# Performance work log

Hardware: AMD Instinct MI355X
Metric: run time of the kernel (lower is better)

## Reference

```python
import jax, jax.numpy as jnp
import numpy as np

B, N, D = 4, 1024, 1024
H, HD, G = 16, 64, 4          # num_heads, dim_heads, num_groups
KVH = H // G                   # kv heads = 4


def setup_inputs() -> dict:
    key = jax.random.key(0)
    ks = jax.random.split(key, 5)
    s = 0.02
    return {
        "x": jax.random.normal(ks[0], (B, N, D), jnp.float32),
        "Wq": jax.random.normal(ks[1], (D, H * HD), jnp.float32) * s,
        "Wkv": jax.random.normal(ks[2], (D, 2 * H * HD // G), jnp.float32) * s,
        "Wg": jax.random.normal(ks[3], (D, H * HD), jnp.float32) * s,
        "bg": jnp.zeros((H * HD,), jnp.float32),
        "Wo": jax.random.normal(ks[4], (H * HD, D), jnp.float32) * s,
    }


def reference(x, Wq, Wkv, Wg, bg, Wo):
    # QKV projections (no bias on q/kv/o; bias on gate)
    q = (x @ Wq).reshape(B, N, H, HD).transpose(0, 2, 1, 3)        # (B,H,N,HD)
    kv = x @ Wkv                                                    # (B,N,2*KVH*HD)
    k, v = jnp.split(kv, 2, axis=-1)
    k = k.reshape(B, N, KVH, HD).transpose(0, 2, 1, 3)             # (B,KVH,N,HD)
    v = v.reshape(B, N, KVH, HD).transpose(0, 2, 1, 3)
    # GQA: repeat_interleave kv heads to match query heads
    k = jnp.repeat(k, G, axis=1)                                    # (B,H,N,HD)
    v = jnp.repeat(v, G, axis=1)
    # scaled dot product attention
    scores = jnp.einsum("bhqd,bhkd->bhqk", q, k) / jnp.sqrt(jnp.float32(HD))
    attn = jax.nn.softmax(scores, axis=-1)
    out = jnp.einsum("bhqk,bhkd->bhqd", attn, v)                    # (B,H,N,HD)
    out = out.transpose(0, 2, 1, 3).reshape(B, N, H * HD)
    # elementwise gate then output projection
    gate = x @ Wg + bg
    return (gate * out) @ Wo
```

## Files before the change

### kernel.cpp

```cpp
#include <hip/hip_runtime.h>
#include <hip/hip_bf16.h>
#include <stdint.h>

#define BB 4
#define NN 1024
#define DD 1024
#define HH 16
#define HDIM 64
#define KVHH 4
#define MM (BB * NN)

typedef __hip_bfloat16 bf16;
typedef __attribute__((ext_vector_type(8))) short bf16x8;
typedef __attribute__((ext_vector_type(4))) short bf16x4;
typedef __attribute__((ext_vector_type(4))) float f32x4;

__device__ __forceinline__ float b2f(unsigned short u) {
  return __uint_as_float(((unsigned)u) << 16);
}
__device__ __forceinline__ unsigned short f2b(float x) {
  bf16 h = __float2bfloat16(x);
  unsigned short u;
  __builtin_memcpy(&u, &h, 2);
  return u;
}
__device__ __forceinline__ f32x4 mfma16(bf16x8 a, bf16x8 b, f32x4 c) {
  return __builtin_amdgcn_mfma_f32_16x16x32_bf16(a, b, c, 0, 0, 0);
}
__device__ __forceinline__ f32x4 mfma16k16(bf16x4 a, bf16x4 b, f32x4 c) {
#if __has_builtin(__builtin_amdgcn_mfma_f32_16x16x16bf16_1k)
  return __builtin_amdgcn_mfma_f32_16x16x16bf16_1k(a, b, c, 0, 0, 0);
#else
  asm("s_nop 1\n\tv_mfma_f32_16x16x16_bf16 %0, %1, %2, %0"
      : "+v"(c)
      : "v"(a), "v"(b));
  return c;
#endif
}
__device__ __forceinline__ bf16x4 vlo(bf16x8 v) {
  return __builtin_shufflevector(v, v, 0, 1, 2, 3);
}
__device__ __forceinline__ bf16x4 vhi(bf16x8 v) {
  return __builtin_shufflevector(v, v, 4, 5, 6, 7);
}
__device__ __forceinline__ void gl_lds16(const short* g, short* l) {
  __builtin_amdgcn_global_load_lds(
      (const __attribute__((address_space(1))) unsigned*)g,
      (__attribute__((address_space(3))) unsigned*)l, 16, 0, 0);
}

__global__ __launch_bounds__(256) void transpose_all(
    const float* __restrict__ Wq, const float* __restrict__ Wkv,
    const float* __restrict__ Wg, const float* __restrict__ Wo,
    const float* __restrict__ bg, const float* __restrict__ x,
    short* __restrict__ WcT, short* __restrict__ WoT,
    float* __restrict__ bias, short* __restrict__ xb) {
  const int z = blockIdx.z;
  if (z == 4) {
    if (blockIdx.y == 0 && blockIdx.x < 10) {
      int i = blockIdx.x * 256 + threadIdx.x;
      if (i < 2560) bias[i] = (i >= 1024 && i < 2048) ? bg[i - 1024] : 0.f;
    }
    return;
  }
  if (z == 5) {
    int base = (blockIdx.y * 16 + blockIdx.x) * 256 + threadIdx.x;
#pragma unroll
    for (int it = 0; it < 16; ++it) {
      int i = base + it * 65536;
      float4 v = *(const float4*)&x[(size_t)i * 4];
      ushort4 o;
      o.x = f2b(v.x); o.y = f2b(v.y); o.z = f2b(v.z); o.w = f2b(v.w);
      *(ushort4*)&xb[(size_t)i * 4] = o;
    }
    return;
  }
  const float* W;
  short* WT;
  int N = 1024;
  const int K = 1024;
  if (z == 0) { W = Wq; WT = WcT; }
  else if (z == 1) { W = Wg; WT = WcT + 1048576; }
  else if (z == 2) {
    W = Wkv; WT = WcT + 2097152; N = 512;
    if (blockIdx.x >= 8) return;
  } else { W = Wo; WT = WoT; }

  __shared__ short T[64 * 68];
  const int tid = threadIdx.x;
  const int n0 = blockIdx.x * 64, k0 = blockIdx.y * 64;
  {
    int i0 = tid >> 4, j4 = (tid & 15) * 4;
#pragma unroll
    for (int ii = 0; ii < 4; ++ii) {
      int i = i0 + 16 * ii;
      float4 w = *(const float4*)&W[(size_t)(k0 + i) * N + n0 + j4];
      ushort4 o;
      o.x = f2b(w.x); o.y = f2b(w.y); o.z = f2b(w.z); o.w = f2b(w.w);
      *(ushort4*)&T[i * 68 + j4] = o;
    }
  }
  __syncthreads();
  {
    int n = tid >> 2, k16 = (tid & 3) * 16;
    short tmp[16];
#pragma unroll
    for (int kk = 0; kk < 16; ++kk) tmp[kk] = T[(k16 + kk) * 68 + n];
    short* dst = WT + (size_t)(n0 + n) * K + k0 + k16;
#pragma unroll
    for (int s = 0; s < 16; s += 4) *(ushort4*)&dst[s] = *(const ushort4*)&tmp[s];
  }
}

__global__ __launch_bounds__(256, 3) void gemm_proj(
    const short* __restrict__ A, const short* __restrict__ WT,
    const float* __restrict__ bias, short* __restrict__ qc,
    short* __restrict__ gc, short* __restrict__ kc, short* __restrict__ vt) {
  __shared__ short As[2][128 * 32];
  __shared__ short Bs[2][128 * 32];
  const int tid = threadIdx.x;
  const int wave = tid >> 6, lane = tid & 63, l15 = lane & 15, quad = lane >> 4;
  const int m0 = blockIdx.y * 128, n0 = blockIdx.x * 128;
  const int wm = (wave & 1) * 64, wn = (wave >> 1) * 64;
  const int arow = tid >> 2, ac = (tid & 3) * 8;
  const short* asrc = A + (size_t)(m0 + arow) * 1024 + ac;
  const short* bsrc = WT + (size_t)(n0 + arow) * 1024 + ac;

  gl_lds16(asrc, &As[0][wave * 512]);
  gl_lds16(asrc + 64 * 1024, &As[0][2048 + wave * 512]);
  gl_lds16(bsrc, &Bs[0][wave * 512]);
  gl_lds16(bsrc + 64 * 1024, &Bs[0][2048 + wave * 512]);

  f32x4 acc[4][4] = {};
  for (int k = 0; k < 32; ++k) {
    const int cur = k & 1;
    __syncthreads();
    if (k < 31) {
      const short* ap = asrc + (k + 1) * 32;
      const short* bp = bsrc + (k + 1) * 32;
      gl_lds16(ap, &As[1 - cur][wave * 512]);
      gl_lds16(ap + 64 * 1024, &As[1 - cur][2048 + wave * 512]);
      gl_lds16(bp, &Bs[1 - cur][wave * 512]);
      gl_lds16(bp + 64 * 1024, &Bs[1 - cur][2048 + wave * 512]);
    }
    bf16x8 af[4], bfr[4];
#pragma unroll
    for (int i = 0; i < 4; ++i)
      af[i] = *(const bf16x8*)&As[cur][(wm + 16 * i + l15) * 32 + quad * 8];
#pragma unroll
    for (int j = 0; j < 4; ++j)
      bfr[j] = *(const bf16x8*)&Bs[cur][(wn + 16 * j + l15) * 32 + quad * 8];
#pragma unroll
    for (int i = 0; i < 4; ++i)
#pragma unroll
      for (int j = 0; j < 4; ++j) acc[i][j] = mfma16(af[i], bfr[j], acc[i][j]);
  }

  const int reg = (n0 + wn) >> 6;
  if (reg < 16) {
#pragma unroll
    for (int j = 0; j < 4; ++j) {
      int d = 16 * j + l15;
#pragma unroll
      for (int i = 0; i < 4; ++i)
#pragma unroll
        for (int r = 0; r < 4; ++r) {
          int row = m0 + wm + 16 * i + quad * 4 + r;
          int b = row >> 10, tok = row & 1023;
          ((unsigned short*)qc)[((size_t)((b * 16 + reg) * 1024 + tok)) * 64 + d] =
              f2b(acc[i][j][r] * 0.18033688f);
        }
    }
  } else if (reg < 32) {
#pragma unroll
    for (int j = 0; j < 4; ++j) {
      int d = 16 * j + l15;
      float bv = bias[n0 + wn + d];
#pragma unroll
      for (int i = 0; i < 4; ++i)
#pragma unroll
        for (int r = 0; r < 4; ++r) {
          int row = m0 + wm + 16 * i + quad * 4 + r;
          int b = row >> 10, tok = row & 1023;
          ((unsigned short*)gc)[((size_t)((b * 16 + reg - 16) * 1024 + tok)) * 64 + d] =
              f2b(acc[i][j][r] + bv);
        }
    }
  } else if (reg < 36) {
    int kvh = reg - 32;
#pragma unroll
    for (int j = 0; j < 4; ++j) {
      int d = 16 * j + l15;
      int dh = d >> 5, dq = (d >> 3) & 3, di = d & 7;
#pragma unroll
      for (int i = 0; i < 4; ++i)
#pragma unroll
        for (int r = 0; r < 4; ++r) {
          int row = m0 + wm + 16 * i + quad * 4 + r;
          int b = row >> 10, tok = row & 1023;
          int kt = tok >> 6, kh = (tok >> 5) & 1, k32 = tok & 31;
          int ksub = k32 >> 4, kl = k32 & 15;
          size_t koff = (size_t)(b * 4 + kvh) * 65536 +
                        (size_t)((kt * 2 + kh) * 2048 + (ksub * 2 + dh) * 512 +
                                 (dq * 16 + kl) * 8 + di);
          ((unsigned short*)kc)[koff] = f2b(acc[i][j][r]);
        }
    }
  } else {
    int kvh = reg - 36;
#pragma unroll
    for (int j = 0; j < 4; ++j) {
      int dt = j;
#pragma unroll
      for (int i = 0; i < 4; ++i) {
        int row0 = m0 + wm + 16 * i + quad * 4;
        int b = row0 >> 10, tok0 = row0 & 1023;
        int kt = tok0 >> 6, kh = (tok0 >> 5) & 1, isub = (tok0 >> 4) & 1;
        size_t voff = (size_t)(b * 4 + kvh) * 65536 +
                      (size_t)((kt * 2 + kh) * 2048 + (isub * 2 + (dt >> 1)) * 512 +
                               (quad * 16 + l15) * 8 + (dt & 1) * 4);
        ushort4 o;
        o.x = f2b(acc[i][j][0]);
        o.y = f2b(acc[i][j][1]);
        o.z = f2b(acc[i][j][2]);
        o.w = f2b(acc[i][j][3]);
        *(ushort4*)&((unsigned short*)vt)[voff] = o;
      }
    }
  }
}

__global__ __launch_bounds__(256, 4) void gemm_out(
    const short* __restrict__ A, const short* __restrict__ WT,
    float* __restrict__ Cout) {
  __shared__ short As[2][128 * 32];
  __shared__ short Bs[2][64 * 32];
  const int tid = threadIdx.x;
  const int wave = tid >> 6, lane = tid & 63, l15 = lane & 15, quad = lane >> 4;
  const int m0 = blockIdx.y * 128, n0 = blockIdx.x * 64;
  const int wm = (wave & 1) * 64, wn = (wave >> 1) * 32;
  const int arow = tid >> 2, ac = (tid & 3) * 8;
  const short* asrc = A + (size_t)(m0 + arow) * 1024 + ac;
  const short* bsrc = WT + (size_t)(n0 + arow) * 1024 + ac;

  gl_lds16(asrc, &As[0][wave * 512]);
  gl_lds16(asrc + 64 * 1024, &As[0][2048 + wave * 512]);
  gl_lds16(bsrc, &Bs[0][wave * 512]);

  f32x4 acc[4][2] = {};
  for (int k = 0; k < 32; ++k) {
    const int cur = k & 1;
    __syncthreads();
    if (k < 31) {
      const short* ap = asrc + (k + 1) * 32;
      gl_lds16(ap, &As[1 - cur][wave * 512]);
      gl_lds16(ap + 64 * 1024, &As[1 - cur][2048 + wave * 512]);
      gl_lds16(bsrc + (k + 1) * 32, &Bs[1 - cur][wave * 512]);
    }
    bf16x8 af[4], bfr[2];
#pragma unroll
    for (int i = 0; i < 4; ++i)
      af[i] = *(const bf16x8*)&As[cur][(wm + 16 * i + l15) * 32 + quad * 8];
#pragma unroll
    for (int j = 0; j < 2; ++j)
      bfr[j] = *(const bf16x8*)&Bs[cur][(wn + 16 * j + l15) * 32 + quad * 8];
#pragma unroll
    for (int i = 0; i < 4; ++i)
#pragma unroll
      for (int j = 0; j < 2; ++j) acc[i][j] = mfma16(af[i], bfr[j], acc[i][j]);
  }
#pragma unroll
  for (int j = 0; j < 2; ++j) {
    int col = n0 + wn + 16 * j + l15;
#pragma unroll
    for (int i = 0; i < 4; ++i) {
#pragma unroll
      for (int r = 0; r < 4; ++r) {
        int row = m0 + wm + 16 * i + quad * 4 + r;
        Cout[(size_t)row * 1024 + col] = acc[i][j][r];
      }
    }
  }
}

__global__ __launch_bounds__(256, 4) void attn_mfma14(
    const short* __restrict__ qc, const short* __restrict__ gc,
    const short* __restrict__ kc, const short* __restrict__ vt,
    unsigned short* __restrict__ gated) {
  __shared__ float OA[64 * 33];
  __shared__ float OB[64 * 33];
  __shared__ float Lpart[4 * 32];
  __shared__ float Lq[64];
  const int tid = threadIdx.x;
  const int w = tid >> 6, lane = tid & 63, l15 = lane & 15, quad = lane >> 4;
  const int qh = w >> 1, kh = w & 1;
  const int qt = blockIdx.x, bh = blockIdx.y, b = bh >> 4, h = bh & 15, kvh = h >> 2;

  bf16x8 qf[2][2];
#pragma unroll
  for (int jq = 0; jq < 2; ++jq) {
    const short* qp = qc + ((size_t)((b * 16 + h) * 1024) + qt * 64 + qh * 32 +
                            16 * jq + l15) * 64 + quad * 8;
    qf[jq][0] = *(const bf16x8*)qp;
    qf[jq][1] = *(const bf16x8*)(qp + 32);
  }

  const short* kp = kc + (size_t)(b * 4 + kvh) * 65536 + kh * 2048 + lane * 8;
  const short* vp = vt + (size_t)(b * 4 + kvh) * 65536 + kh * 2048 + lane * 8;

  f32x4 oacc[2][4] = {};
  float ls[2] = {0.f, 0.f};

  bf16x8 kA0 = *(const bf16x8*)(kp);
  bf16x8 kA1 = *(const bf16x8*)(kp + 512);
  bf16x8 kA2 = *(const bf16x8*)(kp + 1024);
  bf16x8 kA3 = *(const bf16x8*)(kp + 1536);
  bf16x8 w0 = *(const bf16x8*)(vp);
  bf16x8 w1 = *(const bf16x8*)(vp + 512);
  bf16x8 w2 = *(const bf16x8*)(vp + 1024);
  bf16x8 w3 = *(const bf16x8*)(vp + 1536);

#define EXPPV8(ST, JQ, WA, WB)                                                 \
  {                                                                            \
    float p0 = exp2f((ST)[0]), p1 = exp2f((ST)[1]);                            \
    float p2 = exp2f((ST)[2]), p3 = exp2f((ST)[3]);                            \
    ls[JQ] += (p0 + p1) + (p2 + p3);                                           \
    bf16x4 pbf;                                                                \
    pbf[0] = (short)f2b(p0);                                                   \
    pbf[1] = (short)f2b(p1);                                                   \
    pbf[2] = (short)f2b(p2);                                                   \
    pbf[3] = (short)f2b(p3);                                                   \
    oacc[JQ][0] = mfma16k16(vlo(WA), pbf, oacc[JQ][0]);                        \
    oacc[JQ][1] = mfma16k16(vhi(WA), pbf, oacc[JQ][1]);                        \
    oacc[JQ][2] = mfma16k16(vlo(WB), pbf, oacc[JQ][2]);                        \
    oacc[JQ][3] = mfma16k16(vhi(WB), pbf, oacc[JQ][3]);                        \
  }

  for (int kt = 0; kt < 16; ++kt) {
    const short* kn = kp + 4096;
    const short* vn = vp + 4096;
    f32x4 s00 = mfma16(kA0, qf[0][0], (f32x4){0.f, 0.f, 0.f, 0.f});
    s00 = mfma16(kA1, qf[0][1], s00);
    f32x4 s10 = mfma16(kA0, qf[1][0], (f32x4){0.f, 0.f, 0.f, 0.f});
    s10 = mfma16(kA1, qf[1][1], s10);
    if (kt < 15) {
      kA0 = *(const bf16x8*)(kn);
      kA1 = *(const bf16x8*)(kn + 512);
    }
    EXPPV8(s00, 0, w0, w1);
    EXPPV8(s10, 1, w0, w1);
    f32x4 s01 = mfma16(kA2, qf[0][0], (f32x4){0.f, 0.f, 0.f, 0.f});
    s01 = mfma16(kA3, qf[0][1], s01);
    f32x4 s11 = mfma16(kA2, qf[1][0], (f32x4){0.f, 0.f, 0.f, 0.f});
    s11 = mfma16(kA3, qf[1][1], s11);
    if (kt < 15) {
      kA2 = *(const bf16x8*)(kn + 1024);
      kA3 = *(const bf16x8*)(kn + 1536);
    }
    EXPPV8(s01, 0, w2, w3);
    EXPPV8(s11, 1, w2, w3);
    if (kt < 15) {
      w0 = *(const bf16x8*)(vn);
      w1 = *(const bf16x8*)(vn + 512);
      w2 = *(const bf16x8*)(vn + 1024);
      w3 = *(const bf16x8*)(vn + 1536);
    }
    kp = kn;
    vp = vn;
  }
#undef EXPPV8

#pragma unroll
  for (int jq = 0; jq < 2; ++jq) {
    ls[jq] += __shfl_xor(ls[jq], 16);
    ls[jq] += __shfl_xor(ls[jq], 32);
  }
  if (quad == 0) {
#pragma unroll
    for (int jq = 0; jq < 2; ++jq) Lpart[w * 32 + 16 * jq + l15] = ls[jq];
  }

  float* Ob = qh ? OB : OA;
  if (kh == 0) {
#pragma unroll
    for (int jq = 0; jq < 2; ++jq)
#pragma unroll
      for (int dt = 0; dt < 4; ++dt)
#pragma unroll
        for (int r = 0; r < 4; ++r)
          Ob[(16 * dt + 4 * quad + r) * 33 + 16 * jq + l15] = oacc[jq][dt][r];
  }
  __syncthreads();
  if (kh == 1) {
#pragma unroll
    for (int jq = 0; jq < 2; ++jq)
#pragma unroll
      for (int dt = 0; dt < 4; ++dt)
#pragma unroll
        for (int r = 0; r < 4; ++r)
          Ob[(16 * dt + 4 * quad + r) * 33 + 16 * jq + l15] += oacc[jq][dt][r];
  }
  if (tid < 64) {
    int ql = tid & 31, qh2 = tid >> 5;
    Lq[tid] = Lpart[qh2 * 64 + ql] + Lpart[qh2 * 64 + 32 + ql];
  }
  __syncthreads();

  const int d = 16 * w + l15;
#pragma unroll
  for (int jq = 0; jq < 4; ++jq) {
    const float* Osrc = (jq < 2) ? OA : OB;
#pragma unroll
    for (int r = 0; r < 4; ++r) {
      int qloc = 16 * jq + 4 * quad + r;
      float ov = Osrc[d * 33 + (qloc & 31)];
      float lv = Lq[qloc];
      float gv = b2f(((const unsigned short*)gc)[
          ((size_t)((b * 16 + h) * 1024) + qt * 64 + qloc) * 64 + d]);
      size_t row = (size_t)(b * NN + qt * 64 + qloc);
      gated[row * 1024 + h * 64 + d] = f2b(ov / lv * gv);
    }
  }
}

extern "C" void kernel_launch(void* const* d_in, const int* in_sizes, int n_in,
                              void* d_out, int out_size, void* d_ws,
                              size_t ws_size, hipStream_t stream) {
  const float* x = (const float*)d_in[0];
  const float* Wq = (const float*)d_in[1];
  const float* Wkv = (const float*)d_in[2];
  const float* Wg = (const float*)d_in[3];
  const float* bg = (const float*)d_in[4];
  const float* Wo = (const float*)d_in[5];
  float* out = (float*)d_out;

  short* ws = (short*)d_ws;
  short* xb = ws;
  short* WcT = xb + 4194304;
  short* WoT = WcT + 2621440;
  short* qc = WoT + 1048576;
  short* gc = qc + 4194304;
  short* kc = gc + 4194304;
  short* vtw = kc + 1048576;
  float* bias_f32 = (float*)(vtw + 1048576);

  dim3 blk(256);
  transpose_all<<<dim3(16, 16, 6), blk, 0, stream>>>(Wq, Wkv, Wg, Wo, bg, x,
                                                     WcT, WoT, bias_f32, xb);
  gemm_proj<<<dim3(20, 32), blk, 0, stream>>>(xb, WcT, bias_f32, qc, gc, kc, vtw);
  attn_mfma14<<<dim3(16, 64), blk, 0, stream>>>(qc, gc, kc, vtw, (unsigned short*)xb);
  gemm_out<<<dim3(16, 32), blk, 0, stream>>>(xb, WoT, out);
}
```

Baseline: 166.7 us.

## Stage K/V tiles through LDS and swizzle block order across kernels

```diff
diff --git a/kernel.cpp b/kernel.cpp
--- a/kernel.cpp
+++ b/kernel.cpp
@@ -120,7 +120,10 @@
   __shared__ short Bs[2][128 * 32];
   const int tid = threadIdx.x;
   const int wave = tid >> 6, lane = tid & 63, l15 = lane & 15, quad = lane >> 4;
-  const int m0 = blockIdx.y * 128, n0 = blockIdx.x * 128;
+  const int bid0 = blockIdx.x + blockIdx.y * 20;
+  const int swz = (bid0 & 7) * 80 + (bid0 >> 3);
+  const int bx = swz % 20, by = swz / 20;
+  const int m0 = by * 128, n0 = bx * 128;
   const int wm = (wave & 1) * 64, wn = (wave >> 1) * 64;
   const int arow = tid >> 2, ac = (tid & 3) * 8;
   const short* asrc = A + (size_t)(m0 + arow) * 1024 + ac;
@@ -237,7 +240,9 @@
   __shared__ short Bs[2][64 * 32];
   const int tid = threadIdx.x;
   const int wave = tid >> 6, lane = tid & 63, l15 = lane & 15, quad = lane >> 4;
-  const int m0 = blockIdx.y * 128, n0 = blockIdx.x * 64;
+  const int bid0 = blockIdx.x + blockIdx.y * 16;
+  const int swz = (bid0 & 7) * 64 + (bid0 >> 3);
+  const int m0 = (swz >> 4) * 128, n0 = (swz & 15) * 64;
   const int wm = (wave & 1) * 64, wn = (wave >> 1) * 32;
   const int arow = tid >> 2, ac = (tid & 3) * 8;
   const short* asrc = A + (size_t)(m0 + arow) * 1024 + ac;
@@ -283,18 +288,22 @@
   }
 }
 
-__global__ __launch_bounds__(256, 4) void attn_mfma14(
+__global__ __launch_bounds__(256, 4) void attn_mfma15(
     const short* __restrict__ qc, const short* __restrict__ gc,
     const short* __restrict__ kc, const short* __restrict__ vt,
     unsigned short* __restrict__ gated) {
-  __shared__ float OA[64 * 33];
-  __shared__ float OB[64 * 33];
+  __shared__ short KV[2][8192];
   __shared__ float Lpart[4 * 32];
   __shared__ float Lq[64];
+  float* OA = (float*)&KV[0][0];
+  float* OB = OA + 64 * 33;
   const int tid = threadIdx.x;
   const int w = tid >> 6, lane = tid & 63, l15 = lane & 15, quad = lane >> 4;
   const int qh = w >> 1, kh = w & 1;
-  const int qt = blockIdx.x, bh = blockIdx.y, b = bh >> 4, h = bh & 15, kvh = h >> 2;
+  const int bid0 = blockIdx.x + blockIdx.y * 16;
+  const int swz = (bid0 & 7) * 128 + (bid0 >> 3);
+  const int qt = swz & 15, bh = swz >> 4;
+  const int b = bh >> 4, h = bh & 15, kvh = h >> 2;
 
   bf16x8 qf[2][2];
 #pragma unroll
@@ -305,20 +314,22 @@
     qf[jq][1] = *(const bf16x8*)(qp + 32);
   }
 
-  const short* kp = kc + (size_t)(b * 4 + kvh) * 65536 + kh * 2048 + lane * 8;
-  const short* vp = vt + (size_t)(b * 4 + kvh) * 65536 + kh * 2048 + lane * 8;
+  const short* kbase = kc + (size_t)(b * 4 + kvh) * 65536;
+  const short* vbase = vt + (size_t)(b * 4 + kvh) * 65536;
+  const int wdst = w * 512;
+
+#define STAGE(CUR, KT)                                                         \
+  {                                                                            \
+    const short* ks = kbase + (size_t)(KT) * 4096;                             \
+    const short* vs = vbase + (size_t)(KT) * 4096;                             \
+    gl_lds16(ks + tid * 8, &KV[CUR][wdst]);                                    \
+    gl_lds16(ks + 2048 + tid * 8, &KV[CUR][2048 + wdst]);                      \
+    gl_lds16(vs + tid * 8, &KV[CUR][4096 + wdst]);                             \
+    gl_lds16(vs + 2048 + tid * 8, &KV[CUR][6144 + wdst]);                      \
+  }
 
   f32x4 oacc[2][4] = {};
   float ls[2] = {0.f, 0.f};
-
-  bf16x8 kA0 = *(const bf16x8*)(kp);
-  bf16x8 kA1 = *(const bf16x8*)(kp + 512);
-  bf16x8 kA2 = *(const bf16x8*)(kp + 1024);
-  bf16x8 kA3 = *(const bf16x8*)(kp + 1536);
-  bf16x8 w0 = *(const bf16x8*)(vp);
-  bf16x8 w1 = *(const bf16x8*)(vp + 512);
-  bf16x8 w2 = *(const bf16x8*)(vp + 1024);
-  bf16x8 w3 = *(const bf16x8*)(vp + 1536);
 
 #define EXPPV8(ST, JQ, WA, WB)                                                 \
   {                                                                            \
@@ -336,50 +347,47 @@
     oacc[JQ][3] = mfma16k16(vhi(WB), pbf, oacc[JQ][3]);                        \
   }
 
+  STAGE(0, 0);
   for (int kt = 0; kt < 16; ++kt) {
-    const short* kn = kp + 4096;
-    const short* vn = vp + 4096;
+    const int cur = kt & 1;
+    __syncthreads();
+    if (kt < 15) STAGE(cur ^ 1, kt + 1);
+    const short* kl = &KV[cur][kh * 2048 + lane * 8];
+    const short* vl = &KV[cur][4096 + kh * 2048 + lane * 8];
+    bf16x8 kA0 = *(const bf16x8*)(kl);
+    bf16x8 kA1 = *(const bf16x8*)(kl + 512);
+    bf16x8 kA2 = *(const bf16x8*)(kl + 1024);
+    bf16x8 kA3 = *(const bf16x8*)(kl + 1536);
+    bf16x8 w0 = *(const bf16x8*)(vl);
+    bf16x8 w1 = *(const bf16x8*)(vl + 512);
+    bf16x8 w2 = *(const bf16x8*)(vl + 1024);
+    bf16x8 w3 = *(const bf16x8*)(vl + 1536);
     f32x4 s00 = mfma16(kA0, qf[0][0], (f32x4){0.f, 0.f, 0.f, 0.f});
     s00 = mfma16(kA1, qf[0][1], s00);
     f32x4 s10 = mfma16(kA0, qf[1][0], (f32x4){0.f, 0.f, 0.f, 0.f});
     s10 = mfma16(kA1, qf[1][1], s10);
-    if (kt < 15) {
-      kA0 = *(const bf16x8*)(kn);
-      kA1 = *(const bf16x8*)(kn + 512);
-    }
     EXPPV8(s00, 0, w0, w1);
     EXPPV8(s10, 1, w0, w1);
     f32x4 s01 = mfma16(kA2, qf[0][0], (f32x4){0.f, 0.f, 0.f, 0.f});
     s01 = mfma16(kA3, qf[0][1], s01);
     f32x4 s11 = mfma16(kA2, qf[1][0], (f32x4){0.f, 0.f, 0.f, 0.f});
     s11 = mfma16(kA3, qf[1][1], s11);
-    if (kt < 15) {
-      kA2 = *(const bf16x8*)(kn + 1024);
-      kA3 = *(const bf16x8*)(kn + 1536);
-    }
     EXPPV8(s01, 0, w2, w3);
     EXPPV8(s11, 1, w2, w3);
-    if (kt < 15) {
-      w0 = *(const bf16x8*)(vn);
-      w1 = *(const bf16x8*)(vn + 512);
-      w2 = *(const bf16x8*)(vn + 1024);
-      w3 = *(const bf16x8*)(vn + 1536);
-    }
-    kp = kn;
-    vp = vn;
   }
 #undef EXPPV8
+#undef STAGE
 
 #pragma unroll
   for (int jq = 0; jq < 2; ++jq) {
     ls[jq] += __shfl_xor(ls[jq], 16);
     ls[jq] += __shfl_xor(ls[jq], 32);
   }
+  __syncthreads();
   if (quad == 0) {
 #pragma unroll
     for (int jq = 0; jq < 2; ++jq) Lpart[w * 32 + 16 * jq + l15] = ls[jq];
   }
-
   float* Ob = qh ? OB : OA;
   if (kh == 0) {
 #pragma unroll
@@ -448,6 +456,6 @@
   transpose_all<<<dim3(16, 16, 6), blk, 0, stream>>>(Wq, Wkv, Wg, Wo, bg, x,
                                                      WcT, WoT, bias_f32, xb);
   gemm_proj<<<dim3(20, 32), blk, 0, stream>>>(xb, WcT, bias_f32, qc, gc, kc, vtw);
-  attn_mfma14<<<dim3(16, 64), blk, 0, stream>>>(qc, gc, kc, vtw, (unsigned short*)xb);
+  attn_mfma15<<<dim3(16, 64), blk, 0, stream>>>(qc, gc, kc, vtw, (unsigned short*)xb);
   gemm_out<<<dim3(16, 32), blk, 0, stream>>>(xb, WoT, out);
 }
```

Measured after the change: 167.0 us. Within noise of the previous version (+0.2%).
